# Performance work log

Measured on AMD Instinct MI355X. Metric: run time of the kernel, lower is better.

Reference implementation:

```python
import jax, jax.numpy as jnp
import numpy as np

B = 4096      # batch
D = 256       # flattened input feature dim
NUMFEAT = 1 + D + D * (D + 1) // 2  # 33153: bias + linear + quadratic terms


def setup_inputs() -> dict:
    key = jax.random.key(0)
    k1, k2 = jax.random.split(key)
    x = jax.random.normal(k1, (B, D), dtype=jnp.float32)
    # nn.Linear(numfeat, 10, bias=False): weight shape (10, numfeat)
    W = jax.random.normal(k2, (10, NUMFEAT), dtype=jnp.float32) * 0.01
    return {"x": x, "W": W}


def reference(x, W):
    # x: (B, D) -- original does x.view(B, -1); already 2D here.
    b, d = x.shape
    # sklearn PolynomialFeatures(degree=2) column order:
    # [1, x_0..x_{d-1}, x_0*x_0, x_0*x_1, ..., x_{d-1}*x_{d-1}]
    # i.e. combinations_with_replacement == upper-triangular (incl. diagonal)
    iu0, iu1 = np.triu_indices(d)  # static index constants
    ones = jnp.ones((b, 1), dtype=x.dtype)
    cross = x[:, iu0] * x[:, iu1]          # (B, D*(D+1)/2)
    feats = jnp.concatenate([ones, x, cross], axis=1)  # (B, NUMFEAT)
    return feats @ W.T                      # (B, 10)
```

## Files before the change

kernel.cpp:

```cpp
#include <hip/hip_runtime.h>


#define DD 256
#define NF 33153
#define TPB 256
#define ASTRIDE 264

typedef __attribute__((ext_vector_type(8))) short short8;
typedef __attribute__((ext_vector_type(4))) float floatx4;
typedef __attribute__((ext_vector_type(4), aligned(4))) float float4a;

union S8U { unsigned u[4]; short8 s; };

__device__ inline unsigned pack2(float lo, float hi) {
    unsigned a = __builtin_bit_cast(unsigned, hi) + 0x8000u;
    unsigned b = __builtin_bit_cast(unsigned, lo) + 0x8000u;
    return __builtin_amdgcn_perm(a, b, 0x07060302u);
}

__device__ inline short8 load_pack8(const float* __restrict__ p) {
    float4a v0 = *(const float4a*)p;
    float4a v1 = *(const float4a*)(p + 4);
    S8U r;
    r.u[0] = pack2(v0.x, v0.y); r.u[1] = pack2(v0.z, v0.w);
    r.u[2] = pack2(v1.x, v1.y); r.u[3] = pack2(v1.z, v1.w);
    return r.s;
}

__device__ inline int troff(int i) { return 257 + 255 * i - ((i * (i - 1)) >> 1); }

__global__ __launch_bounds__(TPB, 3)
void PolynomialRegression_75385265979710_kernel(const float* __restrict__ x,
                                                const float* __restrict__ W,
                                                float* __restrict__ out) {
    __shared__ __align__(16) unsigned short As[64 * ASTRIDE];
    __shared__ float red[4 * 64];

    const int tid  = threadIdx.x;
    const int lane = tid & 63, wave = tid >> 6;
    const int ln   = lane & 15, quad = lane >> 4;
    const int q8   = quad * 8;
    const int rowbase = blockIdx.x * 64;
    const int o  = blockIdx.y;
    const int g1 = wave, g2 = 7 - wave;
    const int rem = 8 - wave;

#pragma unroll
    for (int it = 0; it < 8; ++it) {
        int idx = it * 2048 + tid * 8;
        int r = idx >> 8, c = idx & 255;
        const float* src = &x[(rowbase + r) * DD + c];
        float4a v0 = *(const float4a*)src;
        float4a v1 = *(const float4a*)(src + 4);
        S8U p;
        p.u[0] = pack2(v0.x, v0.y); p.u[1] = pack2(v0.z, v0.w);
        p.u[2] = pack2(v1.x, v1.y); p.u[3] = pack2(v1.z, v1.w);
        *(short8*)&As[r * ASTRIDE + c] = p.s;
    }

    const float* __restrict__ Wo = W + o * NF;

    const int offA0 = troff(g1 * 32 + ln)      + q8;
    const int offA1 = troff(g1 * 32 + 16 + ln) + q8;
    const int offB0 = troff(g2 * 32 + ln)      + q8;
    const int offB1 = troff(g2 * 32 + 16 + ln) + q8;

    unsigned mA[4], mB[4];
#pragma unroll
    for (int w2 = 0; w2 < 4; ++w2) {
        mA[w2] = ((q8 + 2 * w2     < ln) ? 0u : 0x0000FFFFu)
               | ((q8 + 2 * w2 + 1 < ln) ? 0u : 0xFFFF0000u);
        mB[w2] = ((q8 + 2 * w2     < 16 + ln) ? 0u : 0x0000FFFFu)
               | ((q8 + 2 * w2 + 1 < 16 + ln) ? 0u : 0xFFFF0000u);
    }

    int iRow[4];
    float w1v[4];
#pragma unroll
    for (int nt = 0; nt < 4; ++nt) {
        int g = (nt < 2) ? g1 : g2;
        iRow[nt] = g * 32 + (nt & 1) * 16 + ln;
        w1v[nt]  = Wo[1 + iRow[nt]];
    }
    const float bias = Wo[0];

    S8U pb0, pb1;
    pb0.s = load_pack8(Wo + offA0 + g1 * 32);
    pb1.s = load_pack8(Wo + offA1 + g1 * 32);

    __syncthreads();

    floatx4 acc[4][4];
#pragma unroll
    for (int mt = 0; mt < 4; ++mt)
#pragma unroll
        for (int nt = 0; nt < 4; ++nt) acc[mt][nt] = (floatx4)0.f;

#pragma unroll
    for (int t = 0; t < 9; ++t) {
        const bool first = (t < rem);
        const int kc = first ? (g1 + t) : (g2 + (t - rem));
        const int co = kc * 32;
        S8U b0, b1;
        if (t == 0) {
            b0 = pb0; b1 = pb1;
        } else {
            b0.s = load_pack8(Wo + (first ? offA0 : offB0) + co);
            b1.s = load_pack8(Wo + (first ? offA1 : offB1) + co);
        }
        if (t == 0 || t == rem) {
#pragma unroll
            for (int w2 = 0; w2 < 4; ++w2) { b0.u[w2] &= mA[w2]; b1.u[w2] &= mB[w2]; }
        }
        short8 a[4];
#pragma unroll
        for (int mt = 0; mt < 4; ++mt)
            a[mt] = *(const short8*)&As[(mt * 16 + ln) * ASTRIDE + co + q8];
        if (first) {
#pragma unroll
            for (int mt = 0; mt < 4; ++mt) {
                acc[mt][0] = __builtin_amdgcn_mfma_f32_16x16x32_bf16(a[mt], b0.s, acc[mt][0], 0, 0, 0);
                acc[mt][1] = __builtin_amdgcn_mfma_f32_16x16x32_bf16(a[mt], b1.s, acc[mt][1], 0, 0, 0);
            }
        } else {
#pragma unroll
            for (int mt = 0; mt < 4; ++mt) {
                acc[mt][2] = __builtin_amdgcn_mfma_f32_16x16x32_bf16(a[mt], b0.s, acc[mt][2], 0, 0, 0);
                acc[mt][3] = __builtin_amdgcn_mfma_f32_16x16x32_bf16(a[mt], b1.s, acc[mt][3], 0, 0, 0);
            }
        }
    }

#pragma unroll
    for (int mt = 0; mt < 4; ++mt) {
#pragma unroll
        for (int r = 0; r < 4; ++r) {
            const int m = mt * 16 + quad * 4 + r;
            float p = 0.f;
#pragma unroll
            for (int nt = 0; nt < 4; ++nt) {
                unsigned u = As[m * ASTRIDE + iRow[nt]];
                float xv = __builtin_bit_cast(float, u << 16);
                p = fmaf(xv, acc[mt][nt][r] + w1v[nt], p);
            }
            p += __shfl_xor(p, 1);
            p += __shfl_xor(p, 2);
            p += __shfl_xor(p, 4);
            p += __shfl_xor(p, 8);
            if (ln == 0) red[wave * 64 + m] = p;
        }
    }
    __syncthreads();

    if (tid < 64) {
        float s = red[tid] + red[64 + tid] + red[128 + tid] + red[192 + tid]
                + bias;
        out[(rowbase + tid) * 10 + o] = s;
    }
}

extern "C" void kernel_launch(void* const* d_in, const int* in_sizes, int n_in,
                              void* d_out, int out_size, void* d_ws, size_t ws_size,
                              hipStream_t stream) {
    const float* x = (const float*)d_in[0];
    const float* W = (const float*)d_in[1];
    float* out = (float*)d_out;

    dim3 grid(4096 / 64, 10);
    PolynomialRegression_75385265979710_kernel<<<grid, TPB, 0, stream>>>(x, W, out);
}
```

Baseline: 69.78 us.

## Process two output columns per block to reuse staged x tile

Each block now handles two output columns instead of one, halving the grid in the y dimension. The x tile is loaded and converted to bf16 in shared memory once and reused for both output columns, which removes duplicated global x reads and packing work. The first W chunk for the second column is prefetched after the first column's MFMA loop. In exchange the grid drops from 640 to 320 blocks, which lowers parallelism across CUs, and an extra barrier is added per output column.

```diff
diff --git a/kernel.cpp b/kernel.cpp
--- a/kernel.cpp
+++ b/kernel.cpp
@@ -4,6 +4,7 @@
 #define DD 256
 #define NF 33153
 #define TPB 256
+#define MROWS 64
 #define ASTRIDE 264
 
 typedef __attribute__((ext_vector_type(8))) short short8;
@@ -33,15 +34,15 @@
 void PolynomialRegression_75385265979710_kernel(const float* __restrict__ x,
                                                 const float* __restrict__ W,
                                                 float* __restrict__ out) {
-    __shared__ __align__(16) unsigned short As[64 * ASTRIDE];
-    __shared__ float red[4 * 64];
+    __shared__ __align__(16) unsigned short As[MROWS * ASTRIDE];
+    __shared__ float red[4 * MROWS];
 
     const int tid  = threadIdx.x;
     const int lane = tid & 63, wave = tid >> 6;
     const int ln   = lane & 15, quad = lane >> 4;
     const int q8   = quad * 8;
-    const int rowbase = blockIdx.x * 64;
-    const int o  = blockIdx.y;
+    const int rowbase = blockIdx.x * MROWS;
+    const int o0 = blockIdx.y * 2;
     const int g1 = wave, g2 = 7 - wave;
     const int rem = 8 - wave;
 
@@ -58,8 +59,6 @@
         *(short8*)&As[r * ASTRIDE + c] = p.s;
     }
 
-    const float* __restrict__ Wo = W + o * NF;
-
     const int offA0 = troff(g1 * 32 + ln)      + q8;
     const int offA1 = troff(g1 * 32 + 16 + ln) + q8;
     const int offB0 = troff(g2 * 32 + ln)      + q8;
@@ -75,87 +74,102 @@
     }
 
     int iRow[4];
-    float w1v[4];
 #pragma unroll
     for (int nt = 0; nt < 4; ++nt) {
         int g = (nt < 2) ? g1 : g2;
         iRow[nt] = g * 32 + (nt & 1) * 16 + ln;
-        w1v[nt]  = Wo[1 + iRow[nt]];
     }
-    const float bias = Wo[0];
 
     S8U pb0, pb1;
-    pb0.s = load_pack8(Wo + offA0 + g1 * 32);
-    pb1.s = load_pack8(Wo + offA1 + g1 * 32);
+    pb0.s = load_pack8(W + o0 * NF + offA0 + g1 * 32);
+    pb1.s = load_pack8(W + o0 * NF + offA1 + g1 * 32);
 
     __syncthreads();
 
-    floatx4 acc[4][4];
 #pragma unroll
-    for (int mt = 0; mt < 4; ++mt)
+    for (int oo = 0; oo < 2; ++oo) {
+        const int o = o0 + oo;
+        const float* __restrict__ Wo = W + o * NF;
+
+        float w1v[4];
 #pragma unroll
-        for (int nt = 0; nt < 4; ++nt) acc[mt][nt] = (floatx4)0.f;
+        for (int nt = 0; nt < 4; ++nt) w1v[nt] = Wo[1 + iRow[nt]];
+        const float bias = Wo[0];
+
+        floatx4 acc[4][4];
+#pragma unroll
+        for (int mt = 0; mt < 4; ++mt)
+#pragma unroll
+            for (int nt = 0; nt < 4; ++nt) acc[mt][nt] = (floatx4)0.f;
 
 #pragma unroll
-    for (int t = 0; t < 9; ++t) {
-        const bool first = (t < rem);
-        const int kc = first ? (g1 + t) : (g2 + (t - rem));
-        const int co = kc * 32;
-        S8U b0, b1;
-        if (t == 0) {
-            b0 = pb0; b1 = pb1;
-        } else {
-            b0.s = load_pack8(Wo + (first ? offA0 : offB0) + co);
-            b1.s = load_pack8(Wo + (first ? offA1 : offB1) + co);
-        }
-        if (t == 0 || t == rem) {
+        for (int t = 0; t < 9; ++t) {
+            const bool first = (t < rem);
+            const int kc = first ? (g1 + t) : (g2 + (t - rem));
+            const int co = kc * 32;
+            S8U b0, b1;
+            if (t == 0) {
+                b0 = pb0; b1 = pb1;
+            } else {
+                b0.s = load_pack8(Wo + (first ? offA0 : offB0) + co);
+                b1.s = load_pack8(Wo + (first ? offA1 : offB1) + co);
+            }
+            if (t == 0 || t == rem) {
 #pragma unroll
-            for (int w2 = 0; w2 < 4; ++w2) { b0.u[w2] &= mA[w2]; b1.u[w2] &= mB[w2]; }
-        }
-        short8 a[4];
+                for (int w2 = 0; w2 < 4; ++w2) { b0.u[w2] &= mA[w2]; b1.u[w2] &= mB[w2]; }
+            }
+            short8 a[4];
 #pragma unroll
-        for (int mt = 0; mt < 4; ++mt)
-            a[mt] = *(const short8*)&As[(mt * 16 + ln) * ASTRIDE + co + q8];
-        if (first) {
+            for (int mt = 0; mt < 4; ++mt)
+                a[mt] = *(const short8*)&As[(mt * 16 + ln) * ASTRIDE + co + q8];
+            if (first) {
 #pragma unroll
-            for (int mt = 0; mt < 4; ++mt) {
-                acc[mt][0] = __builtin_amdgcn_mfma_f32_16x16x32_bf16(a[mt], b0.s, acc[mt][0], 0, 0, 0);
-                acc[mt][1] = __builtin_amdgcn_mfma_f32_16x16x32_bf16(a[mt], b1.s, acc[mt][1], 0, 0, 0);
-            }
-        } else {
+                for (int mt = 0; mt < 4; ++mt) {
+                    acc[mt][0] = __builtin_amdgcn_mfma_f32_16x16x32_bf16(a[mt], b0.s, acc[mt][0], 0, 0, 0);
+                    acc[mt][1] = __builtin_amdgcn_mfma_f32_16x16x32_bf16(a[mt], b1.s, acc[mt][1], 0, 0, 0);
+                }
+            } else {
 #pragma unroll
-            for (int mt = 0; mt < 4; ++mt) {
-                acc[mt][2] = __builtin_amdgcn_mfma_f32_16x16x32_bf16(a[mt], b0.s, acc[mt][2], 0, 0, 0);
-                acc[mt][3] = __builtin_amdgcn_mfma_f32_16x16x32_bf16(a[mt], b1.s, acc[mt][3], 0, 0, 0);
+                for (int mt = 0; mt < 4; ++mt) {
+                    acc[mt][2] = __builtin_amdgcn_mfma_f32_16x16x32_bf16(a[mt], b0.s, acc[mt][2], 0, 0, 0);
+                    acc[mt][3] = __builtin_amdgcn_mfma_f32_16x16x32_bf16(a[mt], b1.s, acc[mt][3], 0, 0, 0);
+                }
             }
         }
-    }
+
+        if (oo == 0) {
+            pb0.s = load_pack8(W + (o0 + 1) * NF + offA0 + g1 * 32);
+            pb1.s = load_pack8(W + (o0 + 1) * NF + offA1 + g1 * 32);
+        }
 
 #pragma unroll
-    for (int mt = 0; mt < 4; ++mt) {
+        for (int mt = 0; mt < 4; ++mt) {
 #pragma unroll
-        for (int r = 0; r < 4; ++r) {
-            const int m = mt * 16 + quad * 4 + r;
-            float p = 0.f;
+            for (int r = 0; r < 4; ++r) {
+                const int m = mt * 16 + quad * 4 + r;
+                float p = 0.f;
 #pragma unroll
-            for (int nt = 0; nt < 4; ++nt) {
-                unsigned u = As[m * ASTRIDE + iRow[nt]];
-                float xv = __builtin_bit_cast(float, u << 16);
-                p = fmaf(xv, acc[mt][nt][r] + w1v[nt], p);
+                for (int nt = 0; nt < 4; ++nt) {
+                    unsigned u = As[m * ASTRIDE + iRow[nt]];
+                    float xv = __builtin_bit_cast(float, u << 16);
+                    p = fmaf(xv, acc[mt][nt][r] + w1v[nt], p);
+                }
+                p += __shfl_xor(p, 1);
+                p += __shfl_xor(p, 2);
+                p += __shfl_xor(p, 4);
+                p += __shfl_xor(p, 8);
+                if (ln == 0) red[wave * MROWS + m] = p;
             }
-            p += __shfl_xor(p, 1);
-            p += __shfl_xor(p, 2);
-            p += __shfl_xor(p, 4);
-            p += __shfl_xor(p, 8);
-            if (ln == 0) red[wave * 64 + m] = p;
         }
-    }
-    __syncthreads();
+        __syncthreads();
 
-    if (tid < 64) {
-        float s = red[tid] + red[64 + tid] + red[128 + tid] + red[192 + tid]
-                + bias;
-        out[(rowbase + tid) * 10 + o] = s;
+        if (tid < MROWS) {
+            float s = bias;
+#pragma unroll
+            for (int w = 0; w < 4; ++w) s += red[w * MROWS + tid];
+            out[(rowbase + tid) * 10 + o] = s;
+        }
+        __syncthreads();
     }
 }
 
@@ -166,6 +180,6 @@
     const float* W = (const float*)d_in[1];
     float* out = (float*)d_out;
 
-    dim3 grid(4096 / 64, 10);
+    dim3 grid(4096 / MROWS, 5);
     PolynomialRegression_75385265979710_kernel<<<grid, TPB, 0, stream>>>(x, W, out);
 }
```

After: 81.80 us. 17.2% more time.

## Share staged x tile across two outputs per block with 512 threads

Applied to the files above, without the earlier changes.

Each block now handles two output columns with eight waves, four per output, over the same bf16 x tile in shared memory. This halves the grid in the output dimension, so each x tile is loaded and converted half as often. The W prefetch is also moved ahead of the x staging loop so the two loads overlap. The cost is larger blocks, a different occupancy hint, and fewer blocks in total (320), which may underfill the GPU.

```diff
diff --git a/kernel.cpp b/kernel.cpp
--- a/kernel.cpp
+++ b/kernel.cpp
@@ -3,7 +3,8 @@
 
 #define DD 256
 #define NF 33153
-#define TPB 256
+#define TPB 512
+#define MROWS 64
 #define ASTRIDE 264
 
 typedef __attribute__((ext_vector_type(8))) short short8;
@@ -29,25 +30,39 @@
 
 __device__ inline int troff(int i) { return 257 + 255 * i - ((i * (i - 1)) >> 1); }
 
-__global__ __launch_bounds__(TPB, 3)
+__global__ __launch_bounds__(TPB, 4)
 void PolynomialRegression_75385265979710_kernel(const float* __restrict__ x,
                                                 const float* __restrict__ W,
                                                 float* __restrict__ out) {
-    __shared__ __align__(16) unsigned short As[64 * ASTRIDE];
-    __shared__ float red[4 * 64];
+    __shared__ __align__(16) unsigned short As[MROWS * ASTRIDE];
+    __shared__ float red[2 * 4 * MROWS];
 
     const int tid  = threadIdx.x;
     const int lane = tid & 63, wave = tid >> 6;
+    const int op   = wave >> 2;
+    const int w4   = wave & 3;
     const int ln   = lane & 15, quad = lane >> 4;
     const int q8   = quad * 8;
-    const int rowbase = blockIdx.x * 64;
-    const int o  = blockIdx.y;
-    const int g1 = wave, g2 = 7 - wave;
-    const int rem = 8 - wave;
+    const int rowbase = blockIdx.x * MROWS;
+    const int o0 = blockIdx.y * 2;
+    const int o  = o0 + op;
+    const int g1 = w4, g2 = 7 - w4;
+    const int rem = 8 - w4;
+
+    const float* __restrict__ Wo = W + o * NF;
+
+    const int offA0 = troff(g1 * 32 + ln)      + q8;
+    const int offA1 = troff(g1 * 32 + 16 + ln) + q8;
+    const int offB0 = troff(g2 * 32 + ln)      + q8;
+    const int offB1 = troff(g2 * 32 + 16 + ln) + q8;
+
+    S8U pb0, pb1;
+    pb0.s = load_pack8(Wo + offA0 + g1 * 32);
+    pb1.s = load_pack8(Wo + offA1 + g1 * 32);
 
 #pragma unroll
-    for (int it = 0; it < 8; ++it) {
-        int idx = it * 2048 + tid * 8;
+    for (int it = 0; it < 4; ++it) {
+        int idx = it * 4096 + tid * 8;
         int r = idx >> 8, c = idx & 255;
         const float* src = &x[(rowbase + r) * DD + c];
         float4a v0 = *(const float4a*)src;
@@ -57,13 +72,6 @@
         p.u[2] = pack2(v1.x, v1.y); p.u[3] = pack2(v1.z, v1.w);
         *(short8*)&As[r * ASTRIDE + c] = p.s;
     }
-
-    const float* __restrict__ Wo = W + o * NF;
-
-    const int offA0 = troff(g1 * 32 + ln)      + q8;
-    const int offA1 = troff(g1 * 32 + 16 + ln) + q8;
-    const int offB0 = troff(g2 * 32 + ln)      + q8;
-    const int offB1 = troff(g2 * 32 + 16 + ln) + q8;
 
     unsigned mA[4], mB[4];
 #pragma unroll
@@ -82,11 +90,6 @@
         iRow[nt] = g * 32 + (nt & 1) * 16 + ln;
         w1v[nt]  = Wo[1 + iRow[nt]];
     }
-    const float bias = Wo[0];
-
-    S8U pb0, pb1;
-    pb0.s = load_pack8(Wo + offA0 + g1 * 32);
-    pb1.s = load_pack8(Wo + offA1 + g1 * 32);
 
     __syncthreads();
 
@@ -147,15 +150,17 @@
             p += __shfl_xor(p, 2);
             p += __shfl_xor(p, 4);
             p += __shfl_xor(p, 8);
-            if (ln == 0) red[wave * 64 + m] = p;
+            if (ln == 0) red[op * 4 * MROWS + w4 * MROWS + m] = p;
         }
     }
     __syncthreads();
 
-    if (tid < 64) {
-        float s = red[tid] + red[64 + tid] + red[128 + tid] + red[192 + tid]
-                + bias;
-        out[(rowbase + tid) * 10 + o] = s;
+    if (tid < 2 * MROWS) {
+        const int op2 = tid >> 6, m2 = tid & 63;
+        float s = W[(o0 + op2) * NF];
+#pragma unroll
+        for (int w = 0; w < 4; ++w) s += red[op2 * 4 * MROWS + w * MROWS + m2];
+        out[(rowbase + m2) * 10 + o0 + op2] = s;
     }
 }
 
@@ -166,6 +171,6 @@
     const float* W = (const float*)d_in[1];
     float* out = (float*)d_out;
 
-    dim3 grid(4096 / 64, 10);
+    dim3 grid(4096 / MROWS, 5);
     PolynomialRegression_75385265979710_kernel<<<grid, TPB, 0, stream>>>(x, W, out);
 }
```

Result: slower. 72.85 us (+4.4%).
